# Kernel optimization log

Measured on AMD Instinct MI355X. Metric: run time of the kernel, lower is better.

Reference implementation:

```python
import jax, jax.numpy as jnp
import numpy as np

N, E, G, D, L = 100000, 1600000, 64, 128, 4
CLS_HID, NUM_CLASSES = 256, 10
BN_EPS = 1e-5


def setup_inputs() -> dict:
    key = jax.random.key(0)
    ks = jax.random.split(key, 16)
    s = 0.05
    cls_in = D + L * D  # sum(dims) = 640
    return {
        "node_deg": jax.random.randint(ks[0], (N,), 0, D),
        "edge_index": jax.random.randint(ks[1], (2, E), 0, N),
        "batch_vec": jnp.sort(jax.random.randint(ks[2], (N,), 0, G)),
        "eps": jnp.zeros((L,), jnp.float32),  # GINConv train_eps init 0
        "W1": jax.random.normal(ks[3], (L, D, D), jnp.float32) * s,
        "b1": jax.random.normal(ks[4], (L, D), jnp.float32) * s,
        "W2": jax.random.normal(ks[5], (L, D, D), jnp.float32) * s,
        "b2": jax.random.normal(ks[6], (L, D), jnp.float32) * s,
        "bn_g": jnp.ones((L, D), jnp.float32),
        "bn_b": jnp.zeros((L, D), jnp.float32),
        "Wc1": jax.random.normal(ks[7], (cls_in, CLS_HID), jnp.float32) * s,
        "bc1": jax.random.normal(ks[8], (CLS_HID,), jnp.float32) * s,
        "Wc2": jax.random.normal(ks[9], (CLS_HID, NUM_CLASSES), jnp.float32) * s,
        "bc2": jax.random.normal(ks[10], (NUM_CLASSES,), jnp.float32) * s,
    }


def reference(node_deg, edge_index, batch_vec, eps, W1, b1, W2, b2, bn_g, bn_b, Wc1, bc1, Wc2, bc2):
    n = node_deg.shape[0]
    src, dst = edge_index[0], edge_index[1]
    # OneHotEmbedding of node degree -> initial node features [N, D]
    x = jax.nn.one_hot(node_deg, D, dtype=jnp.float32)
    zs = [x]
    for l in range(eps.shape[0]):
        h_in = zs[-1]
        # GINConv: (1+eps)*x + scatter-add of neighbor features
        agg = jax.ops.segment_sum(h_in[src], dst, num_segments=n)
        h = (1.0 + eps[l]) * h_in + agg
        # mlp: lin -> lrelu -> lin
        h = jax.nn.leaky_relu(h @ W1[l] + b1[l])
        h = h @ W2[l] + b2[l]
        # BatchNorm1d over nodes (training-mode batch stats, biased var)
        mean = h.mean(axis=0)
        var = h.var(axis=0)
        h = (h - mean) * jax.lax.rsqrt(var + BN_EPS) * bn_g[l] + bn_b[l]
        zs.append(jax.nn.leaky_relu(h))
    z = jnp.concatenate(zs, axis=1)  # [N, 640]
    pooled = jax.ops.segment_sum(z, batch_vec, num_segments=G)  # global_add_pool
    pooled = jax.nn.leaky_relu(pooled)
    # classifier head: Linear -> LeakyReLU -> Linear (drop_out=0)
    h = jax.nn.leaky_relu(pooled @ Wc1 + bc1)
    return h @ Wc2 + bc2
```

## Files before the change

kernel.cpp:

```cpp
#include <hip/hip_runtime.h>
#include <hip/hip_bf16.h>


#define N_NODES   100000
#define N_EDGES   1600000
#define N_GRAPHS  64
#define DIM       128
#define N_LAYERS  4
#define CLS_IN    640
#define CLS_HID   256
#define N_CLASSES 10
#define LRELU_SLOPE 0.01f
#define BN_EPS_F    1e-5f

#define NBUCK    782
#define BUCK_CAP 4096

typedef __attribute__((ext_vector_type(8))) short bf16x8;
typedef __attribute__((ext_vector_type(4))) float f32x4;

__device__ __forceinline__ float lrelu(float x) { return x > 0.f ? x : LRELU_SLOPE * x; }

__device__ __forceinline__ uint pack2(float x, float y) {
    uint a = __float_as_uint(x), b = __float_as_uint(y);
    a = (a + 0x7FFFu + ((a >> 16) & 1u)) >> 16;
    b = (b + 0x7FFFu + ((b >> 16) & 1u)) >> 16;
    return a | (b << 16);
}
__device__ __forceinline__ float2 unpack2(uint v) {
    return make_float2(__uint_as_float(v << 16), __uint_as_float(v & 0xFFFF0000u));
}

__global__ void k_convert_w(const float* __restrict__ W1, const float* __restrict__ W2,
                            ushort* __restrict__ W1t, ushort* __restrict__ W2t) {
    int gid = blockIdx.x * blockDim.x + threadIdx.x;
    if (gid >= 8 * DIM * DIM) return;
    int mat = gid >> 14, idx = gid & 16383;
    int k = idx >> 7, n = idx & 127;
    const float* src = (mat < 4) ? (W1 + mat * DIM * DIM) : (W2 + (mat - 4) * DIM * DIM);
    ushort* dst = (mat < 4) ? (W1t + mat * DIM * DIM) : (W2t + (mat - 4) * DIM * DIM);
    uint a = __float_as_uint(src[k * DIM + n]);
    dst[n * DIM + k] = (ushort)((a + 0x7FFFu + ((a >> 16) & 1u)) >> 16);
}

__global__ void k_build_x(const int* __restrict__ deg, uint* __restrict__ x) {
    int gid = blockIdx.x * blockDim.x + threadIdx.x;
    if (gid >= N_NODES * 64) return;
    int i = gid >> 6, c = gid & 63;
    int d = deg[i];
    uint v = 0;
    if ((d >> 1) == c) v = 0x3F80u << (16 * (d & 1));
    x[gid] = v;
}

__global__ void k_deg_pool(const int* __restrict__ deg, const int* __restrict__ batch,
                           float* __restrict__ pooled) {
    int i = blockIdx.x * blockDim.x + threadIdx.x;
    if (i < N_NODES) atomicAdd(&pooled[batch[i] * CLS_IN + deg[i]], 1.0f);
}

__global__ void __launch_bounds__(1024) k_partition(const int* __restrict__ src,
                                                    const int* __restrict__ dst,
                                                    uint* __restrict__ cursor,
                                                    uint* __restrict__ ebuf) {
    __shared__ uint hist[NBUCK];
    __shared__ uint basev[NBUCK];
    int t = threadIdx.x;
    for (int b = t; b < NBUCK; b += 1024) hist[b] = 0;
    __syncthreads();
    int e0 = blockIdx.x * 16384;
    uint msrc[16], mdst[16], mrank[16];
#pragma unroll
    for (int i = 0; i < 16; ++i) {
        int e = e0 + i * 1024 + t;
        if (e < N_EDGES) {
            msrc[i] = (uint)src[e];
            mdst[i] = (uint)dst[e];
            mrank[i] = atomicAdd(&hist[mdst[i] >> 7], 1u);
        } else mdst[i] = 0xFFFFFFFFu;
    }
    __syncthreads();
    for (int b = t; b < NBUCK; b += 1024) {
        uint c = hist[b];
        basev[b] = c ? (uint)(b * BUCK_CAP) + atomicAdd(&cursor[b], c) : 0u;
    }
    __syncthreads();
#pragma unroll
    for (int i = 0; i < 16; ++i) {
        if (mdst[i] != 0xFFFFFFFFu) {
            uint b = mdst[i] >> 7;
            ebuf[basev[b] + mrank[i]] = ((mdst[i] & 127u) << 17) | msrc[i];
        }
    }
}

__global__ void __launch_bounds__(512) k_agg(const uint* __restrict__ h,
                                             const uint* __restrict__ ebuf,
                                             const uint* __restrict__ cursor,
                                             uint* __restrict__ out,
                                             const float* __restrict__ epsv, int layer) {
    __shared__ uint sortedL[BUCK_CAP];
    __shared__ uint hist[128];
    __shared__ uint startv[129];
    const int t = threadIdx.x, lane = t & 63, wave = t >> 6;
    const int b = blockIdx.x;
    int cnt = (int)cursor[b]; if (cnt > BUCK_CAP) cnt = BUCK_CAP;
    if (t < 128) hist[t] = 0;
    __syncthreads();
    uint ent[8], rank[8];
    const uint* ep = ebuf + b * BUCK_CAP;
#pragma unroll
    for (int k = 0; k < 8; ++k) {
        int i = t + k * 512;
        if (i < cnt) { ent[k] = ep[i]; rank[k] = atomicAdd(&hist[ent[k] >> 17], 1u); }
    }
    __syncthreads();
    if (t < 128) startv[t + 1] = hist[t];
    if (t == 0) startv[0] = 0;
    __syncthreads();
    for (int off = 1; off < 128; off <<= 1) {
        uint add = (t < 128 && t >= off) ? startv[t + 1 - off] : 0u;
        __syncthreads();
        if (t < 128 && t >= off) startv[t + 1] += add;
        __syncthreads();
    }
#pragma unroll
    for (int k = 0; k < 8; ++k) {
        int i = t + k * 512;
        if (i < cnt) sortedL[startv[ent[k] >> 17] + rank[k]] = ent[k];
    }
    __syncthreads();
    const float s = 1.0f + epsv[layer];
    const int node0 = b * 128;
    for (int ri = 0; ri < 16; ++ri) {
        int r = wave * 16 + ri;
        int g = node0 + r;
        if (g >= N_NODES) break;
        int beg = (int)startv[r], end = (int)startv[r + 1];
        float2 own = unpack2(h[g * 64 + lane]);
        float ax = s * own.x, ay = s * own.y;
        int j = beg;
        for (; j + 4 <= end; j += 4) {
            uint u0 = sortedL[j]     & 0x1FFFFu;
            uint u1 = sortedL[j + 1] & 0x1FFFFu;
            uint u2 = sortedL[j + 2] & 0x1FFFFu;
            uint u3 = sortedL[j + 3] & 0x1FFFFu;
            uint h0 = h[u0 * 64 + lane], h1 = h[u1 * 64 + lane];
            uint h2 = h[u2 * 64 + lane], h3 = h[u3 * 64 + lane];
            float2 f0 = unpack2(h0), f1 = unpack2(h1), f2 = unpack2(h2), f3 = unpack2(h3);
            ax += (f0.x + f1.x) + (f2.x + f3.x);
            ay += (f0.y + f1.y) + (f2.y + f3.y);
        }
        for (; j < end; ++j) {
            uint u = sortedL[j] & 0x1FFFFu;
            float2 f = unpack2(h[u * 64 + lane]);
            ax += f.x; ay += f.y;
        }
        out[g * 64 + lane] = pack2(ax, ay);
    }
}

#define GEMM_LDS_BYTES 69632
__global__ void __launch_bounds__(256) k_gemm(const ushort* __restrict__ A,
                                              const ushort* __restrict__ Wt,
                                              const float* __restrict__ bias,
                                              ushort* __restrict__ C,
                                              float* __restrict__ stats,
                                              int do_lrelu) {
    __shared__ char pool[GEMM_LDS_BYTES];
    ushort* As = (ushort*)pool;
    ushort* Ws = (ushort*)(pool + 34816);
    float*  Cs = (float*)pool;
    const int t = threadIdx.x;
    const int row0 = blockIdx.x * 128;
    {
        int r = t >> 1, hh = t & 1;
        uint4* l = (uint4*)(As + r * 136 + hh * 64);
        if (row0 + r < N_NODES) {
            const uint4* g = (const uint4*)(A + (size_t)(row0 + r) * DIM + hh * 64);
#pragma unroll
            for (int k = 0; k < 8; ++k) l[k] = g[k];
        } else {
            uint4 z = make_uint4(0, 0, 0, 0);
#pragma unroll
            for (int k = 0; k < 8; ++k) l[k] = z;
        }
        const uint4* gw = (const uint4*)(Wt + r * DIM + hh * 64);
        uint4* lw = (uint4*)(Ws + r * 136 + hh * 64);
#pragma unroll
        for (int k = 0; k < 8; ++k) lw[k] = gw[k];
    }
    __syncthreads();
    const int lane = t & 63, wave = t >> 6;
    const int q = lane >> 4, m = lane & 15;
    const int R = (wave >> 1) * 64, Cb = (wave & 1) * 64;
    f32x4 acc[4][4] = {};
#pragma unroll
    for (int ks = 0; ks < 4; ++ks) {
        bf16x8 a[4], b[4];
#pragma unroll
        for (int i = 0; i < 4; ++i)
            a[i] = *(const bf16x8*)(As + (R + i * 16 + m) * 136 + ks * 32 + q * 8);
#pragma unroll
        for (int j = 0; j < 4; ++j)
            b[j] = *(const bf16x8*)(Ws + (Cb + j * 16 + m) * 136 + ks * 32 + q * 8);
#pragma unroll
        for (int i = 0; i < 4; ++i)
#pragma unroll
            for (int j = 0; j < 4; ++j)
                acc[i][j] = __builtin_amdgcn_mfma_f32_16x16x32_bf16(a[i], b[j], acc[i][j], 0, 0, 0);
    }
    __syncthreads();
    float biasr[4];
#pragma unroll
    for (int j = 0; j < 4; ++j) biasr[j] = bias[Cb + j * 16 + m];
#pragma unroll
    for (int i = 0; i < 4; ++i)
#pragma unroll
        for (int j = 0; j < 4; ++j)
#pragma unroll
            for (int r = 0; r < 4; ++r)
                Cs[(R + i * 16 + q * 4 + r) * 132 + Cb + j * 16 + m] = acc[i][j][r] + biasr[j];
    __syncthreads();
    if (stats != nullptr && t < DIM) {
        int rows = N_NODES - row0; if (rows > 128) rows = 128;
        float s1 = 0.f, s2 = 0.f;
        for (int r = 0; r < rows; ++r) { float v = Cs[r * 132 + t]; s1 += v; s2 += v * v; }
        atomicAdd(&stats[t], s1);
        atomicAdd(&stats[DIM + t], s2);
    }
    {
        int r = t >> 1, hh = t & 1;
        if (row0 + r < N_NODES) {
            uint4* outp = (uint4*)(C + (size_t)(row0 + r) * DIM + hh * 64);
#pragma unroll
            for (int k = 0; k < 8; ++k) {
                float4 v0 = *(const float4*)(Cs + r * 132 + hh * 64 + k * 8);
                float4 v1 = *(const float4*)(Cs + r * 132 + hh * 64 + k * 8 + 4);
                if (do_lrelu) {
                    v0.x = lrelu(v0.x); v0.y = lrelu(v0.y); v0.z = lrelu(v0.z); v0.w = lrelu(v0.w);
                    v1.x = lrelu(v1.x); v1.y = lrelu(v1.y); v1.z = lrelu(v1.z); v1.w = lrelu(v1.w);
                }
                uint4 o;
                o.x = pack2(v0.x, v0.y); o.y = pack2(v0.z, v0.w);
                o.z = pack2(v1.x, v1.y); o.w = pack2(v1.z, v1.w);
                outp[k] = o;
            }
        }
    }
}

__global__ void k_bn_final(float* __restrict__ stats, const float* __restrict__ bn_g,
                           const float* __restrict__ bn_b, int layer) {
    int f = threadIdx.x;
    float mean = stats[f] * (1.0f / N_NODES);
    float var  = stats[DIM + f] * (1.0f / N_NODES) - mean * mean;
    float inv  = rsqrtf(var + BN_EPS_F);
    float sc = bn_g[layer * DIM + f] * inv;
    float sh = bn_b[layer * DIM + f] - mean * sc;
    stats[f] = sc;
    stats[DIM + f] = sh;
}

#define PROWS 128
__global__ void __launch_bounds__(256) k_bnpool(const uint* __restrict__ src,
                                                uint* __restrict__ dst,
                                                const float* __restrict__ stats,
                                                const int* __restrict__ batch,
                                                float* __restrict__ pooled, int colOff) {
    int c = threadIdx.x & 63;
    int chunk = threadIdx.x >> 6;
    int r0 = blockIdx.x * PROWS + chunk * (PROWS / 4);
    float sc0 = stats[2 * c], sc1 = stats[2 * c + 1];
    float sh0 = stats[DIM + 2 * c], sh1 = stats[DIM + 2 * c + 1];
    int curg = -1;
    float a0 = 0.f, a1 = 0.f;
    for (int i = 0; i < PROWS / 4; ++i) {
        int r = r0 + i;
        if (r >= N_NODES) break;
        float2 v = unpack2(src[r * 64 + c]);
        float x0 = lrelu(v.x * sc0 + sh0);
        float x1 = lrelu(v.y * sc1 + sh1);
        dst[r * 64 + c] = pack2(x0, x1);
        int g = batch[r];
        if (g != curg) {
            if (curg >= 0) {
                atomicAdd(&pooled[curg * CLS_IN + colOff + 2 * c], a0);
                atomicAdd(&pooled[curg * CLS_IN + colOff + 2 * c + 1], a1);
            }
            curg = g; a0 = 0.f; a1 = 0.f;
        }
        a0 += x0; a1 += x1;
    }
    if (curg >= 0) {
        atomicAdd(&pooled[curg * CLS_IN + colOff + 2 * c], a0);
        atomicAdd(&pooled[curg * CLS_IN + colOff + 2 * c + 1], a1);
    }
}

__global__ void __launch_bounds__(256) k_classifier(const float* __restrict__ pooled,
                                                    const float* __restrict__ Wc1,
                                                    const float* __restrict__ bc1,
                                                    const float* __restrict__ Wc2,
                                                    const float* __restrict__ bc2,
                                                    float* __restrict__ out) {
    __shared__ float p[CLS_IN];
    __shared__ float hh[CLS_HID];
    int g = blockIdx.x, t = threadIdx.x;
    for (int j = t; j < CLS_IN; j += 256) p[j] = lrelu(pooled[g * CLS_IN + j]);
    __syncthreads();
    float acc = bc1[t];
    for (int k = 0; k < CLS_IN; ++k) acc += p[k] * Wc1[k * CLS_HID + t];
    hh[t] = lrelu(acc);
    __syncthreads();
    if (t < N_CLASSES) {
        float a2 = bc2[t];
        for (int k = 0; k < CLS_HID; ++k) a2 += hh[k] * Wc2[k * N_CLASSES + t];
        out[g * N_CLASSES + t] = a2;
    }
}

extern "C" void kernel_launch(void* const* d_in, const int* in_sizes, int n_in,
                              void* d_out, int out_size, void* d_ws, size_t ws_size,
                              hipStream_t stream) {
    const int*   deg   = (const int*)d_in[0];
    const int*   edges = (const int*)d_in[1];
    const int*   srcv  = edges;
    const int*   dstv  = edges + N_EDGES;
    const int*   batch = (const int*)d_in[2];
    const float* epsv  = (const float*)d_in[3];
    const float* W1    = (const float*)d_in[4];
    const float* b1    = (const float*)d_in[5];
    const float* W2    = (const float*)d_in[6];
    const float* b2    = (const float*)d_in[7];
    const float* bn_g  = (const float*)d_in[8];
    const float* bn_b  = (const float*)d_in[9];
    const float* Wc1   = (const float*)d_in[10];
    const float* bc1   = (const float*)d_in[11];
    const float* Wc2   = (const float*)d_in[12];
    const float* bc2   = (const float*)d_in[13];

    char* ws = (char*)d_ws;
    const size_t BUFB = (size_t)N_NODES * DIM * 2;
    size_t off = 0;
    ushort* buf0   = (ushort*)(ws + off); off += BUFB;
    ushort* buf1   = (ushort*)(ws + off); off += BUFB;
    ushort* W1t    = (ushort*)(ws + off); off += 4 * DIM * DIM * 2;
    ushort* W2t    = (ushort*)(ws + off); off += 4 * DIM * DIM * 2;
    float*  pooled = (float*)(ws + off);  off += N_GRAPHS * CLS_IN * 4;
    float*  statsA = (float*)(ws + off);  off += 4 * 2 * DIM * 4;
    uint*   cursor = (uint*)(ws + off);   off += (NBUCK + 8) * 4;
    uint*   ebuf   = (uint*)(ws + off);   off += (size_t)NBUCK * BUCK_CAP * 4;

    hipMemsetAsync(pooled, 0, N_GRAPHS * CLS_IN * 4, stream);
    hipMemsetAsync(statsA, 0, 4 * 2 * DIM * 4, stream);
    hipMemsetAsync(cursor, 0, NBUCK * 4, stream);

    k_convert_w<<<(8 * DIM * DIM + 255) / 256, 256, 0, stream>>>(W1, W2, W1t, W2t);
    k_build_x<<<(N_NODES * 64 + 255) / 256, 256, 0, stream>>>(deg, (uint*)buf0);
    k_deg_pool<<<(N_NODES + 255) / 256, 256, 0, stream>>>(deg, batch, pooled);
    k_partition<<<(N_EDGES + 16383) / 16384, 1024, 0, stream>>>(srcv, dstv, cursor, ebuf);

    const int gemm_grid = (N_NODES + 127) / 128;
    for (int l = 0; l < N_LAYERS; ++l) {
        float* stats = statsA + l * 2 * DIM;
        k_agg<<<NBUCK, 512, 0, stream>>>((const uint*)buf0, ebuf, cursor,
                                         (uint*)buf1, epsv, l);
        k_gemm<<<gemm_grid, 256, 0, stream>>>(buf1, W1t + l * DIM * DIM, b1 + l * DIM,
                                              buf1, nullptr, 1);
        k_gemm<<<gemm_grid, 256, 0, stream>>>(buf1, W2t + l * DIM * DIM, b2 + l * DIM,
                                              buf1, stats, 0);
        k_bn_final<<<1, DIM, 0, stream>>>(stats, bn_g, bn_b, l);
        k_bnpool<<<(N_NODES + PROWS - 1) / PROWS, 256, 0, stream>>>(
            (const uint*)buf1, (uint*)buf0, stats, batch, pooled, DIM * (l + 1));
    }

    k_classifier<<<N_GRAPHS, 256, 0, stream>>>(pooled, Wc1, bc1, Wc2, bc2, (float*)d_out);
}
```

Before: 721.5 us.

## Build global CSR once and gather from feature-sliced node layout

```diff
diff --git a/kernel.cpp b/kernel.cpp
--- a/kernel.cpp
+++ b/kernel.cpp
@@ -15,6 +15,7 @@
 
 #define NBUCK    782
 #define BUCK_CAP 4096
+#define SLICE_PITCH (N_NODES * 8)
 
 typedef __attribute__((ext_vector_type(8))) short bf16x8;
 typedef __attribute__((ext_vector_type(4))) float f32x4;
@@ -44,13 +45,14 @@
 }
 
 __global__ void k_build_x(const int* __restrict__ deg, uint* __restrict__ x) {
-    int gid = blockIdx.x * blockDim.x + threadIdx.x;
-    if (gid >= N_NODES * 64) return;
-    int i = gid >> 6, c = gid & 63;
+    int s = blockIdx.y;
+    int idx = blockIdx.x * 256 + threadIdx.x;
+    if (idx >= N_NODES * 8) return;
+    int i = idx >> 3, u = idx & 7;
     int d = deg[i];
-    uint v = 0;
-    if ((d >> 1) == c) v = 0x3F80u << (16 * (d & 1));
-    x[gid] = v;
+    int c = s * 8 + u;
+    uint v = ((d >> 1) == c) ? (0x3F80u << (16 * (d & 1))) : 0u;
+    x[(size_t)s * SLICE_PITCH + idx] = v;
 }
 
 __global__ void k_deg_pool(const int* __restrict__ deg, const int* __restrict__ batch,
@@ -94,16 +96,32 @@
     }
 }
 
-__global__ void __launch_bounds__(512) k_agg(const uint* __restrict__ h,
-                                             const uint* __restrict__ ebuf,
-                                             const uint* __restrict__ cursor,
-                                             uint* __restrict__ out,
-                                             const float* __restrict__ epsv, int layer) {
+__global__ void __launch_bounds__(1024) k_bases(const uint* __restrict__ cursor,
+                                                uint* __restrict__ base,
+                                                int* __restrict__ indptr) {
+    __shared__ uint sh[1024];
+    int t = threadIdx.x;
+    uint v = (t < NBUCK) ? min(cursor[t], (uint)BUCK_CAP) : 0u;
+    sh[t] = v; __syncthreads();
+    for (int off = 1; off < 1024; off <<= 1) {
+        uint add = (t >= off) ? sh[t - off] : 0u;
+        __syncthreads();
+        sh[t] += add;
+        __syncthreads();
+    }
+    if (t < NBUCK) base[t] = sh[t] - v;
+    if (t == NBUCK - 1) indptr[N_NODES] = (int)sh[t];
+}
+
+__global__ void __launch_bounds__(512) k_sort(const uint* __restrict__ ebuf,
+                                              const uint* __restrict__ cursor,
+                                              const uint* __restrict__ base,
+                                              int* __restrict__ csr,
+                                              int* __restrict__ indptr) {
     __shared__ uint sortedL[BUCK_CAP];
     __shared__ uint hist[128];
     __shared__ uint startv[129];
-    const int t = threadIdx.x, lane = t & 63, wave = t >> 6;
-    const int b = blockIdx.x;
+    const int t = threadIdx.x, b = blockIdx.x;
     int cnt = (int)cursor[b]; if (cnt > BUCK_CAP) cnt = BUCK_CAP;
     if (t < 128) hist[t] = 0;
     __syncthreads();
@@ -130,34 +148,48 @@
         if (i < cnt) sortedL[startv[ent[k] >> 17] + rank[k]] = ent[k];
     }
     __syncthreads();
-    const float s = 1.0f + epsv[layer];
-    const int node0 = b * 128;
-    for (int ri = 0; ri < 16; ++ri) {
-        int r = wave * 16 + ri;
-        int g = node0 + r;
-        if (g >= N_NODES) break;
-        int beg = (int)startv[r], end = (int)startv[r + 1];
-        float2 own = unpack2(h[g * 64 + lane]);
-        float ax = s * own.x, ay = s * own.y;
-        int j = beg;
-        for (; j + 4 <= end; j += 4) {
-            uint u0 = sortedL[j]     & 0x1FFFFu;
-            uint u1 = sortedL[j + 1] & 0x1FFFFu;
-            uint u2 = sortedL[j + 2] & 0x1FFFFu;
-            uint u3 = sortedL[j + 3] & 0x1FFFFu;
-            uint h0 = h[u0 * 64 + lane], h1 = h[u1 * 64 + lane];
-            uint h2 = h[u2 * 64 + lane], h3 = h[u3 * 64 + lane];
-            float2 f0 = unpack2(h0), f1 = unpack2(h1), f2 = unpack2(h2), f3 = unpack2(h3);
-            ax += (f0.x + f1.x) + (f2.x + f3.x);
-            ay += (f0.y + f1.y) + (f2.y + f3.y);
-        }
-        for (; j < end; ++j) {
-            uint u = sortedL[j] & 0x1FFFFu;
-            float2 f = unpack2(h[u * 64 + lane]);
-            ax += f.x; ay += f.y;
-        }
-        out[g * 64 + lane] = pack2(ax, ay);
-    }
+    int gbase = (int)base[b];
+    for (int i = t; i < cnt; i += 512)
+        csr[gbase + i] = (int)(sortedL[i] & 0x1FFFFu);
+    if (t < 128) {
+        int node = b * 128 + t;
+        if (node < N_NODES) indptr[node] = gbase + (int)startv[t];
+    }
+}
+
+__global__ void __launch_bounds__(512) k_agg2(const uint* __restrict__ h,
+                                              const int* __restrict__ indptr,
+                                              const int* __restrict__ csr,
+                                              uint* __restrict__ out,
+                                              const float* __restrict__ epsv, int layer) {
+    const int grp = blockIdx.x >> 3, s = blockIdx.x & 7;
+    const int t = threadIdx.x;
+    const int nloc = t >> 3, u = t & 7;
+    const int node = grp * 64 + nloc;
+    if (node >= N_NODES) return;
+    const uint* hs = h + (size_t)s * SLICE_PITCH;
+    const float se = 1.0f + epsv[layer];
+    float2 own = unpack2(hs[node * 8 + u]);
+    float ax = se * own.x, ay = se * own.y;
+    const int beg = indptr[node], end = indptr[node + 1];
+    int j = beg;
+    for (; j + 4 <= end; j += 4) {
+        int i0 = __builtin_nontemporal_load(&csr[j]);
+        int i1 = __builtin_nontemporal_load(&csr[j + 1]);
+        int i2 = __builtin_nontemporal_load(&csr[j + 2]);
+        int i3 = __builtin_nontemporal_load(&csr[j + 3]);
+        uint w0 = hs[i0 * 8 + u], w1 = hs[i1 * 8 + u];
+        uint w2 = hs[i2 * 8 + u], w3 = hs[i3 * 8 + u];
+        float2 f0 = unpack2(w0), f1 = unpack2(w1), f2 = unpack2(w2), f3 = unpack2(w3);
+        ax += (f0.x + f1.x) + (f2.x + f3.x);
+        ay += (f0.y + f1.y) + (f2.y + f3.y);
+    }
+    for (; j < end; ++j) {
+        int i0 = __builtin_nontemporal_load(&csr[j]);
+        float2 f = unpack2(hs[i0 * 8 + u]);
+        ax += f.x; ay += f.y;
+    }
+    __builtin_nontemporal_store(pack2(ax, ay), &out[node * 64 + s * 8 + u]);
 }
 
 #define GEMM_LDS_BYTES 69632
@@ -268,20 +300,21 @@
                                                 const float* __restrict__ stats,
                                                 const int* __restrict__ batch,
                                                 float* __restrict__ pooled, int colOff) {
-    int c = threadIdx.x & 63;
-    int chunk = threadIdx.x >> 6;
-    int r0 = blockIdx.x * PROWS + chunk * (PROWS / 4);
+    int t = threadIdx.x;
+    int s = t >> 5, sub = t & 31, u = sub & 7, ro = sub >> 3;
+    int c = s * 8 + u;
+    int r0 = blockIdx.x * PROWS + ro;
     float sc0 = stats[2 * c], sc1 = stats[2 * c + 1];
     float sh0 = stats[DIM + 2 * c], sh1 = stats[DIM + 2 * c + 1];
     int curg = -1;
     float a0 = 0.f, a1 = 0.f;
     for (int i = 0; i < PROWS / 4; ++i) {
-        int r = r0 + i;
+        int r = r0 + i * 4;
         if (r >= N_NODES) break;
         float2 v = unpack2(src[r * 64 + c]);
         float x0 = lrelu(v.x * sc0 + sh0);
         float x1 = lrelu(v.y * sc1 + sh1);
-        dst[r * 64 + c] = pack2(x0, x1);
+        dst[(size_t)s * SLICE_PITCH + r * 8 + u] = pack2(x0, x1);
         int g = batch[r];
         if (g != curg) {
             if (curg >= 0) {
@@ -350,6 +383,9 @@
     float*  pooled = (float*)(ws + off);  off += N_GRAPHS * CLS_IN * 4;
     float*  statsA = (float*)(ws + off);  off += 4 * 2 * DIM * 4;
     uint*   cursor = (uint*)(ws + off);   off += (NBUCK + 8) * 4;
+    uint*   base   = (uint*)(ws + off);   off += (NBUCK + 8) * 4;
+    int*    indptr = (int*)(ws + off);    off += (N_NODES + 8) * 4;
+    int*    csr    = (int*)(ws + off);    off += (size_t)N_EDGES * 4;
     uint*   ebuf   = (uint*)(ws + off);   off += (size_t)NBUCK * BUCK_CAP * 4;
 
     hipMemsetAsync(pooled, 0, N_GRAPHS * CLS_IN * 4, stream);
@@ -357,15 +393,21 @@
     hipMemsetAsync(cursor, 0, NBUCK * 4, stream);
 
     k_convert_w<<<(8 * DIM * DIM + 255) / 256, 256, 0, stream>>>(W1, W2, W1t, W2t);
-    k_build_x<<<(N_NODES * 64 + 255) / 256, 256, 0, stream>>>(deg, (uint*)buf0);
+    {
+        dim3 gx((N_NODES * 8 + 255) / 256, 8);
+        k_build_x<<<gx, 256, 0, stream>>>(deg, (uint*)buf0);
+    }
     k_deg_pool<<<(N_NODES + 255) / 256, 256, 0, stream>>>(deg, batch, pooled);
     k_partition<<<(N_EDGES + 16383) / 16384, 1024, 0, stream>>>(srcv, dstv, cursor, ebuf);
+    k_bases<<<1, 1024, 0, stream>>>(cursor, base, indptr);
+    k_sort<<<NBUCK, 512, 0, stream>>>(ebuf, cursor, base, csr, indptr);
 
     const int gemm_grid = (N_NODES + 127) / 128;
+    const int agg_grid  = ((N_NODES + 63) / 64) * 8;
     for (int l = 0; l < N_LAYERS; ++l) {
         float* stats = statsA + l * 2 * DIM;
-        k_agg<<<NBUCK, 512, 0, stream>>>((const uint*)buf0, ebuf, cursor,
-                                         (uint*)buf1, epsv, l);
+        k_agg2<<<agg_grid, 512, 0, stream>>>((const uint*)buf0, indptr, csr,
+                                             (uint*)buf1, epsv, l);
         k_gemm<<<gemm_grid, 256, 0, stream>>>(buf1, W1t + l * DIM * DIM, b1 + l * DIM,
                                               buf1, nullptr, 1);
         k_gemm<<<gemm_grid, 256, 0, stream>>>(buf1, W2t + l * DIM * DIM, b2 + l * DIM,
```

Result: slower. 1.127 ms (+56.2%).
